# Performance work log

Hardware: AMD Instinct MI355X
Metric: run time of the kernel (lower is better)

Reference implementation:

```python
import jax, jax.numpy as jnp
import numpy as np

V, E, EH, H = 32000, 512, 1024, 512  # vocab, emb_dim, enc_hidden, dec_hidden
B, S = 16, 128


def setup_inputs() -> dict:
    key = jax.random.key(0)
    ks = jax.random.split(key, 8)
    g = lambda k, shape, scale: (jax.random.normal(k, shape, jnp.float32) * scale)
    return {
        "y": jax.random.randint(ks[0], (B, S), 0, V),
        "hn": jax.random.normal(ks[1], (B, 1, EH), jnp.float32),
        "emb": g(ks[2], (V, E), 0.02),          # embedding table
        "W_ih": g(ks[3], (3 * H, E), 0.05),      # GRU input weights (r,z,n)
        "W_hh": g(ks[4], (3 * H, H), 0.05),      # GRU hidden weights (r,z,n)
        "b_ih": jnp.zeros((3 * H,), jnp.float32),
        "b_hh": jnp.zeros((3 * H,), jnp.float32),
        "fc_w": g(ks[5], (H, EH), 0.03),         # fc: enc_hidden -> dec_hidden
        "fc_b": jnp.zeros((H,), jnp.float32),
        "pred_w": g(ks[6], (V, H), 0.03),        # pred: dec_hidden -> vocab
        "pred_b": jnp.zeros((V,), jnp.float32),
    }


def gru_scan(x, h0, W_ih, W_hh, b_ih, b_hh):
    """Single-layer unidirectional GRU (PyTorch gate order r,z,n).
    x: [B,S,E], h0: [B,H] -> outputs [B,S,H]."""
    h_dim = h0.shape[-1]
    # precompute input projections for all timesteps: [B,S,3H]
    gx = jnp.einsum('bse,ge->bsg', x, W_ih) + b_ih
    Wr, Wz, Wn = W_hh[:h_dim], W_hh[h_dim:2 * h_dim], W_hh[2 * h_dim:]
    br, bz, bn = b_hh[:h_dim], b_hh[h_dim:2 * h_dim], b_hh[2 * h_dim:]

    def step(h, g):
        gr, gz, gn = g[:, :h_dim], g[:, h_dim:2 * h_dim], g[:, 2 * h_dim:]
        r = jax.nn.sigmoid(gr + h @ Wr.T + br)
        z = jax.nn.sigmoid(gz + h @ Wz.T + bz)
        n = jnp.tanh(gn + r * (h @ Wn.T + bn))
        h_new = (1.0 - z) * n + z * h
        return h_new, h_new

    _, outs = jax.lax.scan(step, h0, jnp.swapaxes(gx, 0, 1))  # [S,B,H]
    return jnp.swapaxes(outs, 0, 1)  # [B,S,H]


def reference(y, hn, emb, W_ih, W_hh, b_ih, b_hh, fc_w, fc_b, pred_w, pred_b):
    # hn: [B,1,EH] -> fc -> [B,1,H] -> permute(1,0,2) -> initial hidden [B,H]
    h0 = (hn @ fc_w.T + fc_b)[:, 0, :]
    x = emb[y]  # [B,S,E]; dropout is identity in eval mode
    out = gru_scan(x, h0, W_ih, W_hh, b_ih, b_hh)  # [B,S,H]
    return out @ pred_w.T + pred_b  # [B,S,V]
```

## Files before the change

kernel.cpp:

```cpp
#include <hip/hip_runtime.h>


typedef __attribute__((ext_vector_type(8))) short           bf8_t;
typedef __attribute__((ext_vector_type(8))) unsigned short  us8_t;
typedef __attribute__((ext_vector_type(4))) unsigned short  us4_t;
typedef __attribute__((ext_vector_type(4))) float           f4_t;
typedef __attribute__((ext_vector_type(4))) unsigned int    u4_t;

#define SENT 0xFFFFFFFFu

__device__ __forceinline__ unsigned short f2bf(float x) {
    unsigned u = __builtin_bit_cast(unsigned, x);
    u += 0x7FFFu + ((u >> 16) & 1u);
    return (unsigned short)(u >> 16);
}
__device__ __forceinline__ float bf2f(unsigned short h) {
    unsigned u = (unsigned)h << 16;
    return __builtin_bit_cast(float, u);
}
__device__ __forceinline__ float sigm(float x) { return 1.0f / (1.0f + __expf(-x)); }

__device__ __forceinline__ void llc_store_f32(float* p, float v) {
    asm volatile("global_store_dword %0, %1, off sc0 sc1" :: "v"(p), "v"(v) : "memory");
}

__global__ void k_fill(unsigned int* __restrict__ p) {
    int i = blockIdx.x * blockDim.x + threadIdx.x;
    u4_t v = {SENT, SENT, SENT, SENT};
    ((u4_t*)p)[i] = v;
}

__global__ void k_conv(const float* __restrict__ src, unsigned short* __restrict__ dst, int n4) {
    int i = blockIdx.x * blockDim.x + threadIdx.x;
    int stride = gridDim.x * blockDim.x;
    for (; i < n4; i += stride) {
        f4_t v = ((const f4_t*)src)[i];
        us4_t o;
        o[0] = f2bf(v[0]); o[1] = f2bf(v[1]); o[2] = f2bf(v[2]); o[3] = f2bf(v[3]);
        ((us4_t*)dst)[i] = o;
    }
}

__global__ void k_gather(const int* __restrict__ y, const float* __restrict__ emb,
                         unsigned short* __restrict__ xbf) {
    int m = blockIdx.x;
    int row = y[m];
    int t = threadIdx.x;
    f4_t v = ((const f4_t*)(emb + (size_t)row * 512))[t];
    us4_t o;
    o[0] = f2bf(v[0]); o[1] = f2bf(v[1]); o[2] = f2bf(v[2]); o[3] = f2bf(v[3]);
    ((us4_t*)(xbf + (size_t)m * 512))[t] = o;
}

__global__ void k_h0(const float* __restrict__ hn, const float* __restrict__ fc_w,
                     const float* __restrict__ fc_b, float* __restrict__ h0) {
    __shared__ float sh[1024];
    int b = blockIdx.x, t = threadIdx.x;
    for (int i = t; i < 1024; i += 256) sh[i] = hn[b * 1024 + i];
    __syncthreads();
    int j = t;
    float a0 = fc_b[j], a1 = fc_b[j + 256];
    const float* w0 = fc_w + (size_t)j * 1024;
    const float* w1 = fc_w + (size_t)(j + 256) * 1024;
    #pragma unroll 8
    for (int e = 0; e < 1024; e++) { float he = sh[e]; a0 += he * w0[e]; a1 += he * w1[e]; }
    h0[b * 512 + j] = a0;
    h0[b * 512 + j + 256] = a1;
}

__launch_bounds__(256)
__global__ void k_gemm(const unsigned short* __restrict__ A, const unsigned short* __restrict__ Bt,
                       const float* __restrict__ bias, float* __restrict__ C, int N) {
    __shared__ unsigned short sA[128 * 64];
    __shared__ unsigned short sB[128 * 64];
    const int m0 = blockIdx.y * 128, n0 = blockIdx.x * 128;
    const int tid = threadIdx.x, lane = tid & 63, wave = tid >> 6;
    const int wm = wave >> 1, wn = wave & 1;
    f4_t acc[4][4] = {};
    for (int ks = 0; ks < 8; ks++) {
        const int k0 = ks * 64;
        #pragma unroll
        for (int t = 0; t < 4; t++) {
            int idx = tid + t * 256;
            int row = idx >> 3, slot = idx & 7;
            int sw = ((slot ^ (row & 7)) << 3);
            *(us8_t*)(&sA[row * 64 + sw]) = *(const us8_t*)(A + (size_t)(m0 + row) * 512 + k0 + slot * 8);
            *(us8_t*)(&sB[row * 64 + sw]) = *(const us8_t*)(Bt + (size_t)(n0 + row) * 512 + k0 + slot * 8);
        }
        __syncthreads();
        #pragma unroll
        for (int kk = 0; kk < 2; kk++) {
            bf8_t af[4], bfr[4];
            #pragma unroll
            for (int mi = 0; mi < 4; mi++) {
                int row = wm * 64 + mi * 16 + (lane & 15);
                int slot = (kk * 4 + (lane >> 4)) ^ (row & 7);
                af[mi] = *(const bf8_t*)(&sA[row * 64 + slot * 8]);
            }
            #pragma unroll
            for (int ni = 0; ni < 4; ni++) {
                int row = wn * 64 + ni * 16 + (lane & 15);
                int slot = (kk * 4 + (lane >> 4)) ^ (row & 7);
                bfr[ni] = *(const bf8_t*)(&sB[row * 64 + slot * 8]);
            }
            #pragma unroll
            for (int mi = 0; mi < 4; mi++)
                #pragma unroll
                for (int ni = 0; ni < 4; ni++)
                    acc[mi][ni] = __builtin_amdgcn_mfma_f32_16x16x32_bf16(af[mi], bfr[ni], acc[mi][ni], 0, 0, 0);
        }
        __syncthreads();
    }
    #pragma unroll
    for (int ni = 0; ni < 4; ni++) {
        int col = n0 + wn * 64 + ni * 16 + (lane & 15);
        float bv = bias[col];
        #pragma unroll
        for (int mi = 0; mi < 4; mi++) {
            int rbase = m0 + wm * 64 + mi * 16 + (lane >> 4) * 4;
            #pragma unroll
            for (int r = 0; r < 4; r++)
                C[(size_t)(rbase + r) * N + col] = acc[mi][ni][r] + bv;
        }
    }
}

__launch_bounds__(512, 1)
__global__ void k_rec(const float* __restrict__ W_hh, const float* __restrict__ b_hh,
                      const float* __restrict__ gx, float* __restrict__ hbuf,
                      unsigned short* __restrict__ Hout) {
    const int kb = blockIdx.x;
    const int j0 = kb * 32;
    const int tid = threadIdx.x, lane = tid & 63, wave = tid >> 6;
    __shared__ unsigned short sHi[16 * 512];
    __shared__ unsigned short sLo[16 * 512];
    __shared__ float sPre[96 * 17];

    bf8_t wfrag[16];
    if (wave < 6) {
        const int gate = wave >> 1, sub = wave & 1;
        const int wrow = gate * 512 + j0 + sub * 16 + (lane & 15);
        const f4_t* wp4 = (const f4_t*)(W_hh + (size_t)wrow * 512);
        #pragma unroll
        for (int kk = 0; kk < 16; kk++) {
            f4_t v0 = wp4[kk * 8 + (lane >> 4) * 2];
            f4_t v1 = wp4[kk * 8 + (lane >> 4) * 2 + 1];
            bf8_t f;
            f[0] = (short)f2bf(v0[0]); f[1] = (short)f2bf(v0[1]);
            f[2] = (short)f2bf(v0[2]); f[3] = (short)f2bf(v0[3]);
            f[4] = (short)f2bf(v1[0]); f[5] = (short)f2bf(v1[1]);
            f[6] = (short)f2bf(v1[2]); f[7] = (short)f2bf(v1[3]);
            wfrag[kk] = f;
        }
    }

    const int b_ = tid >> 5, jj = tid & 31;
    const float brv = b_hh[j0 + jj], bzv = b_hh[512 + j0 + jj], bnv = b_hh[1024 + j0 + jj];
    float h_reg = hbuf[b_ * 512 + j0 + jj];

    for (int s = 1; s <= 128; s++) {
        const float* gxp = gx + (size_t)(b_ * 128 + (s - 1)) * 1536 + j0 + jj;
        float gr = gxp[0], gz = gxp[512], gn = gxp[1024];

        const float* hsrc = hbuf + (size_t)(s - 1) * 8192;
        const float* p0 = hsrc + (size_t)tid * 4;
        const float* p1 = hsrc + (size_t)(tid + 512) * 4;
        const float* p2 = hsrc + (size_t)(tid + 1024) * 4;
        const float* p3 = hsrc + (size_t)(tid + 1536) * 4;
        f4_t hv0, hv1, hv2, hv3;
        int spins = 0;
        bool ok;
        do {
            asm volatile(
                "global_load_dwordx4 %0, %4, off sc0 sc1\n\t"
                "global_load_dwordx4 %1, %5, off sc0 sc1\n\t"
                "global_load_dwordx4 %2, %6, off sc0 sc1\n\t"
                "global_load_dwordx4 %3, %7, off sc0 sc1\n\t"
                "s_waitcnt vmcnt(0)"
                : "=&v"(hv0), "=&v"(hv1), "=&v"(hv2), "=&v"(hv3)
                : "v"(p0), "v"(p1), "v"(p2), "v"(p3)
                : "memory");
            ok = true;
            #pragma unroll
            for (int i = 0; i < 4; i++) {
                ok = ok && (__builtin_bit_cast(unsigned, hv0[i]) != SENT)
                        && (__builtin_bit_cast(unsigned, hv1[i]) != SENT)
                        && (__builtin_bit_cast(unsigned, hv2[i]) != SENT)
                        && (__builtin_bit_cast(unsigned, hv3[i]) != SENT);
            }
        } while (!ok && ++spins < (1 << 20));
        __builtin_amdgcn_sched_barrier(0);

        {
            f4_t hv[4] = {hv0, hv1, hv2, hv3};
            #pragma unroll
            for (int t = 0; t < 4; t++) {
                int idx4 = tid + t * 512;
                int row = idx4 >> 7, c4 = idx4 & 127;
                us4_t hi, lo;
                #pragma unroll
                for (int i = 0; i < 4; i++) {
                    unsigned short h = f2bf(hv[t][i]);
                    hi[i] = h;
                    lo[i] = f2bf(hv[t][i] - bf2f(h));
                }
                int base = row * 512 + (((c4 >> 1) ^ (row & 7)) << 3) + (c4 & 1) * 4;
                *(us4_t*)(&sHi[base]) = hi;
                *(us4_t*)(&sLo[base]) = lo;
            }
        }
        __syncthreads();

        if (wave < 6) {
            f4_t acc = {0.f, 0.f, 0.f, 0.f};
            const int m = lane & 15;
            #pragma unroll
            for (int kk = 0; kk < 16; kk++) {
                int off = m * 512 + (((kk * 4 + (lane >> 4)) ^ (m & 7)) << 3);
                bf8_t ahi = *(const bf8_t*)(&sHi[off]);
                bf8_t alo = *(const bf8_t*)(&sLo[off]);
                acc = __builtin_amdgcn_mfma_f32_16x16x32_bf16(ahi, wfrag[kk], acc, 0, 0, 0);
                acc = __builtin_amdgcn_mfma_f32_16x16x32_bf16(alo, wfrag[kk], acc, 0, 0, 0);
            }
            const int n = wave * 16 + (lane & 15);
            #pragma unroll
            for (int r = 0; r < 4; r++) sPre[n * 17 + (lane >> 4) * 4 + r] = acc[r];
        }
        __syncthreads();

        float r = sigm(gr + sPre[jj * 17 + b_] + brv);
        float z = sigm(gz + sPre[(32 + jj) * 17 + b_] + bzv);
        float nn = tanhf(gn + r * (sPre[(64 + jj) * 17 + b_] + bnv));
        float hnew = (1.f - z) * nn + z * h_reg;
        h_reg = hnew;

        llc_store_f32(&hbuf[(size_t)s * 8192 + b_ * 512 + j0 + jj], hnew);
        Hout[(size_t)(b_ * 128 + (s - 1)) * 512 + j0 + jj] = f2bf(hnew);
    }
}

extern "C" void kernel_launch(void* const* d_in, const int* in_sizes, int n_in,
                              void* d_out, int out_size, void* d_ws, size_t ws_size,
                              hipStream_t stream) {
    const int*   y      = (const int*)  d_in[0];
    const float* hn     = (const float*)d_in[1];
    const float* emb    = (const float*)d_in[2];
    const float* W_ih   = (const float*)d_in[3];
    const float* W_hh   = (const float*)d_in[4];
    const float* b_ih   = (const float*)d_in[5];
    const float* b_hh   = (const float*)d_in[6];
    const float* fc_w   = (const float*)d_in[7];
    const float* fc_b   = (const float*)d_in[8];
    const float* pred_w = (const float*)d_in[9];
    const float* pred_b = (const float*)d_in[10];
    float* out = (float*)d_out;

    char* ws = (char*)d_ws;
    size_t off = 0;
    auto alloc = [&](size_t bytes) { void* p = ws + off; off = (off + bytes + 255) & ~(size_t)255; return p; };
    float*          hbuf   = (float*)          alloc((size_t)129 * 8192 * 4);
    float*          gx     = (float*)          alloc((size_t)2048 * 1536 * 4);
    unsigned short* Hout   = (unsigned short*) alloc((size_t)2048 * 512 * 2);
    unsigned short* xbf    = (unsigned short*) alloc((size_t)2048 * 512 * 2);
    unsigned short* wihbf  = (unsigned short*) alloc((size_t)1536 * 512 * 2);
    unsigned short* pwbf   = (unsigned short*) alloc((size_t)32000 * 512 * 2);
    (void)ws_size; (void)in_sizes; (void)n_in; (void)out_size;

    k_fill  <<<1032, 256, 0, stream>>>((unsigned int*)hbuf);
    k_conv  <<<4096, 256, 0, stream>>>(pred_w, pwbf, 32000 * 512 / 4);
    k_conv  <<<512,  256, 0, stream>>>(W_ih,  wihbf, 1536 * 512 / 4);
    k_gather<<<2048, 128, 0, stream>>>(y, emb, xbf);
    k_h0    <<<16,   256, 0, stream>>>(hn, fc_w, fc_b, hbuf);
    dim3 gG(12, 16);
    k_gemm  <<<gG, 256, 0, stream>>>(xbf, wihbf, b_ih, gx, 1536);
    k_rec   <<<16, 512, 0, stream>>>(W_hh, b_hh, gx, hbuf, Hout);
    dim3 gP(250, 16);
    k_gemm  <<<gP, 256, 0, stream>>>(Hout, pwbf, pred_b, out, 32000);
}
```

Before: 572.5 us.

## Fuse all three GRU gates per wave and compute gate math in MFMA registers

Each of the first two waves now holds the r, z and n weight fragments for its 16 hidden columns and issues all six MFMA chains itself, so gate nonlinearities and the hidden update run directly on accumulator registers. This drops the sPre shared buffer and the shared-memory round trip that fed the gate math. It also prefetches the next step's gx values during the current step. The cost is that only 2 waves do the matmul instead of 6, which serialises six times more MFMAs per wave on the critical path and raises register pressure from the three fragment arrays.

```diff
diff --git a/kernel.cpp b/kernel.cpp
--- a/kernel.cpp
+++ b/kernel.cpp
@@ -19,6 +19,15 @@
     return __builtin_bit_cast(float, u);
 }
 __device__ __forceinline__ float sigm(float x) { return 1.0f / (1.0f + __expf(-x)); }
+
+__device__ __forceinline__ bf8_t mk_frag(f4_t v0, f4_t v1) {
+    bf8_t f;
+    f[0] = (short)f2bf(v0[0]); f[1] = (short)f2bf(v0[1]);
+    f[2] = (short)f2bf(v0[2]); f[3] = (short)f2bf(v0[3]);
+    f[4] = (short)f2bf(v1[0]); f[5] = (short)f2bf(v1[1]);
+    f[6] = (short)f2bf(v1[2]); f[7] = (short)f2bf(v1[3]);
+    return f;
+}
 
 __device__ __forceinline__ void llc_store_f32(float* p, float v) {
     asm volatile("global_store_dword %0, %1, off sc0 sc1" :: "v"(p), "v"(v) : "memory");
@@ -134,34 +143,38 @@
     const int tid = threadIdx.x, lane = tid & 63, wave = tid >> 6;
     __shared__ unsigned short sHi[16 * 512];
     __shared__ unsigned short sLo[16 * 512];
-    __shared__ float sPre[96 * 17];
-
-    bf8_t wfrag[16];
-    if (wave < 6) {
-        const int gate = wave >> 1, sub = wave & 1;
-        const int wrow = gate * 512 + j0 + sub * 16 + (lane & 15);
-        const f4_t* wp4 = (const f4_t*)(W_hh + (size_t)wrow * 512);
+
+    const bool comp = (wave < 2);
+    const int cidx = j0 + wave * 16 + (lane & 15);
+    const int bbase = (lane >> 4) * 4;
+
+    bf8_t wfR[16], wfZ[16], wfN[16];
+    float brv = 0.f, bzv = 0.f, bnv = 0.f;
+    f4_t h_reg = {0.f, 0.f, 0.f, 0.f};
+    float gxv[3][4];
+    if (comp) {
+        const f4_t* wr = (const f4_t*)(W_hh + (size_t)cidx * 512);
+        const f4_t* wz = (const f4_t*)(W_hh + (size_t)(512 + cidx) * 512);
+        const f4_t* wn = (const f4_t*)(W_hh + (size_t)(1024 + cidx) * 512);
+        const int fo = (lane >> 4) * 2;
         #pragma unroll
         for (int kk = 0; kk < 16; kk++) {
-            f4_t v0 = wp4[kk * 8 + (lane >> 4) * 2];
-            f4_t v1 = wp4[kk * 8 + (lane >> 4) * 2 + 1];
-            bf8_t f;
-            f[0] = (short)f2bf(v0[0]); f[1] = (short)f2bf(v0[1]);
-            f[2] = (short)f2bf(v0[2]); f[3] = (short)f2bf(v0[3]);
-            f[4] = (short)f2bf(v1[0]); f[5] = (short)f2bf(v1[1]);
-            f[6] = (short)f2bf(v1[2]); f[7] = (short)f2bf(v1[3]);
-            wfrag[kk] = f;
-        }
-    }
-
-    const int b_ = tid >> 5, jj = tid & 31;
-    const float brv = b_hh[j0 + jj], bzv = b_hh[512 + j0 + jj], bnv = b_hh[1024 + j0 + jj];
-    float h_reg = hbuf[b_ * 512 + j0 + jj];
+            wfR[kk] = mk_frag(wr[kk * 8 + fo], wr[kk * 8 + fo + 1]);
+            wfZ[kk] = mk_frag(wz[kk * 8 + fo], wz[kk * 8 + fo + 1]);
+            wfN[kk] = mk_frag(wn[kk * 8 + fo], wn[kk * 8 + fo + 1]);
+        }
+        brv = b_hh[cidx]; bzv = b_hh[512 + cidx]; bnv = b_hh[1024 + cidx];
+        #pragma unroll
+        for (int r = 0; r < 4; r++)
+            h_reg[r] = hbuf[(bbase + r) * 512 + cidx];
+        #pragma unroll
+        for (int g = 0; g < 3; g++)
+            #pragma unroll
+            for (int r = 0; r < 4; r++)
+                gxv[g][r] = gx[(size_t)((bbase + r) * 128) * 1536 + g * 512 + cidx];
+    }
 
     for (int s = 1; s <= 128; s++) {
-        const float* gxp = gx + (size_t)(b_ * 128 + (s - 1)) * 1536 + j0 + jj;
-        float gr = gxp[0], gz = gxp[512], gn = gxp[1024];
-
         const float* hsrc = hbuf + (size_t)(s - 1) * 8192;
         const float* p0 = hsrc + (size_t)tid * 4;
         const float* p1 = hsrc + (size_t)(tid + 512) * 4;
@@ -191,6 +204,16 @@
         } while (!ok && ++spins < (1 << 20));
         __builtin_amdgcn_sched_barrier(0);
 
+        float gnx[3][4];
+        if (comp) {
+            const int si = (s < 128) ? s : 127;
+            #pragma unroll
+            for (int g = 0; g < 3; g++)
+                #pragma unroll
+                for (int r = 0; r < 4; r++)
+                    gnx[g][r] = gx[(size_t)((bbase + r) * 128 + si) * 1536 + g * 512 + cidx];
+        }
+
         {
             f4_t hv[4] = {hv0, hv1, hv2, hv3};
             #pragma unroll
@@ -211,31 +234,39 @@
         }
         __syncthreads();
 
-        if (wave < 6) {
-            f4_t acc = {0.f, 0.f, 0.f, 0.f};
+        if (comp) {
+            f4_t aR = {}, aZ = {}, aN = {}, cR = {}, cZ = {}, cN = {};
             const int m = lane & 15;
             #pragma unroll
             for (int kk = 0; kk < 16; kk++) {
                 int off = m * 512 + (((kk * 4 + (lane >> 4)) ^ (m & 7)) << 3);
                 bf8_t ahi = *(const bf8_t*)(&sHi[off]);
                 bf8_t alo = *(const bf8_t*)(&sLo[off]);
-                acc = __builtin_amdgcn_mfma_f32_16x16x32_bf16(ahi, wfrag[kk], acc, 0, 0, 0);
-                acc = __builtin_amdgcn_mfma_f32_16x16x32_bf16(alo, wfrag[kk], acc, 0, 0, 0);
-            }
-            const int n = wave * 16 + (lane & 15);
-            #pragma unroll
-            for (int r = 0; r < 4; r++) sPre[n * 17 + (lane >> 4) * 4 + r] = acc[r];
+                aR = __builtin_amdgcn_mfma_f32_16x16x32_bf16(ahi, wfR[kk], aR, 0, 0, 0);
+                aZ = __builtin_amdgcn_mfma_f32_16x16x32_bf16(ahi, wfZ[kk], aZ, 0, 0, 0);
+                aN = __builtin_amdgcn_mfma_f32_16x16x32_bf16(ahi, wfN[kk], aN, 0, 0, 0);
+                cR = __builtin_amdgcn_mfma_f32_16x16x32_bf16(alo, wfR[kk], cR, 0, 0, 0);
+                cZ = __builtin_amdgcn_mfma_f32_16x16x32_bf16(alo, wfZ[kk], cZ, 0, 0, 0);
+                cN = __builtin_amdgcn_mfma_f32_16x16x32_bf16(alo, wfN[kk], cN, 0, 0, 0);
+            }
+            #pragma unroll
+            for (int r = 0; r < 4; r++) {
+                const int b = bbase + r;
+                float rr = sigm(gxv[0][r] + (aR[r] + cR[r]) + brv);
+                float zz = sigm(gxv[1][r] + (aZ[r] + cZ[r]) + bzv);
+                float nn = tanhf(gxv[2][r] + rr * ((aN[r] + cN[r]) + bnv));
+                float hnew = (1.f - zz) * nn + zz * h_reg[r];
+                h_reg[r] = hnew;
+                llc_store_f32(&hbuf[(size_t)s * 8192 + b * 512 + cidx], hnew);
+                Hout[(size_t)(b * 128 + (s - 1)) * 512 + cidx] = f2bf(hnew);
+            }
+            #pragma unroll
+            for (int g = 0; g < 3; g++)
+                #pragma unroll
+                for (int r = 0; r < 4; r++)
+                    gxv[g][r] = gnx[g][r];
         }
         __syncthreads();
-
-        float r = sigm(gr + sPre[jj * 17 + b_] + brv);
-        float z = sigm(gz + sPre[(32 + jj) * 17 + b_] + bzv);
-        float nn = tanhf(gn + r * (sPre[(64 + jj) * 17 + b_] + bnv));
-        float hnew = (1.f - z) * nn + z * h_reg;
-        h_reg = hnew;
-
-        llc_store_f32(&hbuf[(size_t)s * 8192 + b_ * 512 + j0 + jj], hnew);
-        Hout[(size_t)(b_ * 128 + (s - 1)) * 512 + j0 + jj] = f2bf(hnew);
     }
 }
 
```

Result: slower. 932.6 us (+62.9%).

## Restructure GRU recurrence to single-wave blocks exchanging packed bf16 hidden state

Applied to the files above, without the earlier changes.

The recurrent kernel changes from 16 blocks of 512 threads to 32 single-wave blocks. Each block owns 16 hidden columns for all three gates, and each wave loads the whole previous hidden state straight from global memory into MFMA fragments, so the LDS staging and both __syncthreads per step go away. The hidden state is now exchanged as packed bf16 pairs instead of fp32, which halves the polling traffic. The hi/lo split-precision MFMA is dropped, so the recurrent matmul runs in plain bf16. This cuts per-step latency in the sequential loop but lowers accuracy of the recurrent state.

```diff
diff --git a/kernel.cpp b/kernel.cpp
--- a/kernel.cpp
+++ b/kernel.cpp
@@ -14,13 +14,18 @@
     u += 0x7FFFu + ((u >> 16) & 1u);
     return (unsigned short)(u >> 16);
 }
-__device__ __forceinline__ float bf2f(unsigned short h) {
-    unsigned u = (unsigned)h << 16;
-    return __builtin_bit_cast(float, u);
-}
 __device__ __forceinline__ float sigm(float x) { return 1.0f / (1.0f + __expf(-x)); }
 
-__device__ __forceinline__ void llc_store_f32(float* p, float v) {
+__device__ __forceinline__ bf8_t mk_frag(f4_t v0, f4_t v1) {
+    bf8_t f;
+    f[0] = (short)f2bf(v0[0]); f[1] = (short)f2bf(v0[1]);
+    f[2] = (short)f2bf(v0[2]); f[3] = (short)f2bf(v0[3]);
+    f[4] = (short)f2bf(v1[0]); f[5] = (short)f2bf(v1[1]);
+    f[6] = (short)f2bf(v1[2]); f[7] = (short)f2bf(v1[3]);
+    return f;
+}
+
+__device__ __forceinline__ void llc_store_u32(unsigned int* p, unsigned int v) {
     asm volatile("global_store_dword %0, %1, off sc0 sc1" :: "v"(p), "v"(v) : "memory");
 }
 
@@ -53,7 +58,7 @@
 }
 
 __global__ void k_h0(const float* __restrict__ hn, const float* __restrict__ fc_w,
-                     const float* __restrict__ fc_b, float* __restrict__ h0) {
+                     const float* __restrict__ fc_b, float* __restrict__ h0m) {
     __shared__ float sh[1024];
     int b = blockIdx.x, t = threadIdx.x;
     for (int i = t; i < 1024; i += 256) sh[i] = hn[b * 1024 + i];
@@ -64,8 +69,8 @@
     const float* w1 = fc_w + (size_t)(j + 256) * 1024;
     #pragma unroll 8
     for (int e = 0; e < 1024; e++) { float he = sh[e]; a0 += he * w0[e]; a1 += he * w1[e]; }
-    h0[b * 512 + j] = a0;
-    h0[b * 512 + j + 256] = a1;
+    h0m[b * 512 + j] = a0;
+    h0m[b * 512 + j + 256] = a1;
 }
 
 __launch_bounds__(256)
@@ -125,117 +130,112 @@
     }
 }
 
-__launch_bounds__(512, 1)
+__launch_bounds__(64, 1)
 __global__ void k_rec(const float* __restrict__ W_hh, const float* __restrict__ b_hh,
-                      const float* __restrict__ gx, float* __restrict__ hbuf,
-                      unsigned short* __restrict__ Hout) {
-    const int kb = blockIdx.x;
-    const int j0 = kb * 32;
-    const int tid = threadIdx.x, lane = tid & 63, wave = tid >> 6;
-    __shared__ unsigned short sHi[16 * 512];
-    __shared__ unsigned short sLo[16 * 512];
-    __shared__ float sPre[96 * 17];
-
-    bf8_t wfrag[16];
-    if (wave < 6) {
-        const int gate = wave >> 1, sub = wave & 1;
-        const int wrow = gate * 512 + j0 + sub * 16 + (lane & 15);
-        const f4_t* wp4 = (const f4_t*)(W_hh + (size_t)wrow * 512);
+                      const float* __restrict__ gx, const float* __restrict__ h0m,
+                      unsigned int* __restrict__ hbuf, unsigned short* __restrict__ Hout) {
+    const int c = blockIdx.x;
+    const int lane = threadIdx.x;
+    const int col = c * 16 + (lane & 15);
+    const int kgrp = lane >> 4;
+    const int bbase = kgrp * 4;
+
+    bf8_t wfR[16], wfZ[16], wfN[16];
+    {
+        const f4_t* wr = (const f4_t*)(W_hh + (size_t)col * 512);
+        const f4_t* wz = (const f4_t*)(W_hh + (size_t)(512 + col) * 512);
+        const f4_t* wn = (const f4_t*)(W_hh + (size_t)(1024 + col) * 512);
+        const int fo = kgrp * 2;
         #pragma unroll
         for (int kk = 0; kk < 16; kk++) {
-            f4_t v0 = wp4[kk * 8 + (lane >> 4) * 2];
-            f4_t v1 = wp4[kk * 8 + (lane >> 4) * 2 + 1];
-            bf8_t f;
-            f[0] = (short)f2bf(v0[0]); f[1] = (short)f2bf(v0[1]);
-            f[2] = (short)f2bf(v0[2]); f[3] = (short)f2bf(v0[3]);
-            f[4] = (short)f2bf(v1[0]); f[5] = (short)f2bf(v1[1]);
-            f[6] = (short)f2bf(v1[2]); f[7] = (short)f2bf(v1[3]);
-            wfrag[kk] = f;
-        }
-    }
-
-    const int b_ = tid >> 5, jj = tid & 31;
-    const float brv = b_hh[j0 + jj], bzv = b_hh[512 + j0 + jj], bnv = b_hh[1024 + j0 + jj];
-    float h_reg = hbuf[b_ * 512 + j0 + jj];
+            wfR[kk] = mk_frag(wr[kk * 8 + fo], wr[kk * 8 + fo + 1]);
+            wfZ[kk] = mk_frag(wz[kk * 8 + fo], wz[kk * 8 + fo + 1]);
+            wfN[kk] = mk_frag(wn[kk * 8 + fo], wn[kk * 8 + fo + 1]);
+        }
+    }
+    const float brv = b_hh[col], bzv = b_hh[512 + col], bnv = b_hh[1024 + col];
+
+    f4_t h_reg;
+    #pragma unroll
+    for (int r = 0; r < 4; r++) h_reg[r] = h0m[(bbase + r) * 512 + col];
+
+    #pragma unroll
+    for (int r = 0; r < 4; r++) {
+        unsigned int hb = f2bf(h_reg[r]);
+        unsigned int pr = __shfl_xor(hb, 1, 64);
+        if (!(lane & 1))
+            llc_store_u32(&hbuf[(bbase + r) * 256 + (col >> 1)], hb | (pr << 16));
+    }
 
     for (int s = 1; s <= 128; s++) {
-        const float* gxp = gx + (size_t)(b_ * 128 + (s - 1)) * 1536 + j0 + jj;
-        float gr = gxp[0], gz = gxp[512], gn = gxp[1024];
-
-        const float* hsrc = hbuf + (size_t)(s - 1) * 8192;
-        const float* p0 = hsrc + (size_t)tid * 4;
-        const float* p1 = hsrc + (size_t)(tid + 512) * 4;
-        const float* p2 = hsrc + (size_t)(tid + 1024) * 4;
-        const float* p3 = hsrc + (size_t)(tid + 1536) * 4;
-        f4_t hv0, hv1, hv2, hv3;
+        float gxr[4], gxz[4], gxn[4];
+        #pragma unroll
+        for (int r = 0; r < 4; r++) {
+            const float* gp = gx + (size_t)((bbase + r) * 128 + (s - 1)) * 1536 + col;
+            gxr[r] = gp[0]; gxz[r] = gp[512]; gxn[r] = gp[1024];
+        }
+
+        const unsigned int* base = hbuf + (size_t)(s - 1) * 4096 + (lane & 15) * 256 + kgrp * 4;
+        u4_t q[16];
         int spins = 0;
         bool ok;
         do {
             asm volatile(
-                "global_load_dwordx4 %0, %4, off sc0 sc1\n\t"
-                "global_load_dwordx4 %1, %5, off sc0 sc1\n\t"
-                "global_load_dwordx4 %2, %6, off sc0 sc1\n\t"
-                "global_load_dwordx4 %3, %7, off sc0 sc1\n\t"
+                "global_load_dwordx4 %0,  %16, off sc0 sc1\n\t"
+                "global_load_dwordx4 %1,  %16, off offset:64 sc0 sc1\n\t"
+                "global_load_dwordx4 %2,  %16, off offset:128 sc0 sc1\n\t"
+                "global_load_dwordx4 %3,  %16, off offset:192 sc0 sc1\n\t"
+                "global_load_dwordx4 %4,  %16, off offset:256 sc0 sc1\n\t"
+                "global_load_dwordx4 %5,  %16, off offset:320 sc0 sc1\n\t"
+                "global_load_dwordx4 %6,  %16, off offset:384 sc0 sc1\n\t"
+                "global_load_dwordx4 %7,  %16, off offset:448 sc0 sc1\n\t"
+                "global_load_dwordx4 %8,  %16, off offset:512 sc0 sc1\n\t"
+                "global_load_dwordx4 %9,  %16, off offset:576 sc0 sc1\n\t"
+                "global_load_dwordx4 %10, %16, off offset:640 sc0 sc1\n\t"
+                "global_load_dwordx4 %11, %16, off offset:704 sc0 sc1\n\t"
+                "global_load_dwordx4 %12, %16, off offset:768 sc0 sc1\n\t"
+                "global_load_dwordx4 %13, %16, off offset:832 sc0 sc1\n\t"
+                "global_load_dwordx4 %14, %16, off offset:896 sc0 sc1\n\t"
+                "global_load_dwordx4 %15, %16, off offset:960 sc0 sc1\n\t"
                 "s_waitcnt vmcnt(0)"
-                : "=&v"(hv0), "=&v"(hv1), "=&v"(hv2), "=&v"(hv3)
-                : "v"(p0), "v"(p1), "v"(p2), "v"(p3)
+                : "=&v"(q[0]), "=&v"(q[1]), "=&v"(q[2]), "=&v"(q[3]),
+                  "=&v"(q[4]), "=&v"(q[5]), "=&v"(q[6]), "=&v"(q[7]),
+                  "=&v"(q[8]), "=&v"(q[9]), "=&v"(q[10]), "=&v"(q[11]),
+                  "=&v"(q[12]), "=&v"(q[13]), "=&v"(q[14]), "=&v"(q[15])
+                : "v"(base)
                 : "memory");
             ok = true;
             #pragma unroll
-            for (int i = 0; i < 4; i++) {
-                ok = ok && (__builtin_bit_cast(unsigned, hv0[i]) != SENT)
-                        && (__builtin_bit_cast(unsigned, hv1[i]) != SENT)
-                        && (__builtin_bit_cast(unsigned, hv2[i]) != SENT)
-                        && (__builtin_bit_cast(unsigned, hv3[i]) != SENT);
-            }
-        } while (!ok && ++spins < (1 << 20));
+            for (int kk = 0; kk < 16; kk++)
+                #pragma unroll
+                for (int i = 0; i < 4; i++)
+                    ok = ok && (q[kk][i] != SENT);
+        } while (!__all(ok) && ++spins < (1 << 20));
         __builtin_amdgcn_sched_barrier(0);
 
-        {
-            f4_t hv[4] = {hv0, hv1, hv2, hv3};
-            #pragma unroll
-            for (int t = 0; t < 4; t++) {
-                int idx4 = tid + t * 512;
-                int row = idx4 >> 7, c4 = idx4 & 127;
-                us4_t hi, lo;
-                #pragma unroll
-                for (int i = 0; i < 4; i++) {
-                    unsigned short h = f2bf(hv[t][i]);
-                    hi[i] = h;
-                    lo[i] = f2bf(hv[t][i] - bf2f(h));
-                }
-                int base = row * 512 + (((c4 >> 1) ^ (row & 7)) << 3) + (c4 & 1) * 4;
-                *(us4_t*)(&sHi[base]) = hi;
-                *(us4_t*)(&sLo[base]) = lo;
-            }
-        }
-        __syncthreads();
-
-        if (wave < 6) {
-            f4_t acc = {0.f, 0.f, 0.f, 0.f};
-            const int m = lane & 15;
-            #pragma unroll
-            for (int kk = 0; kk < 16; kk++) {
-                int off = m * 512 + (((kk * 4 + (lane >> 4)) ^ (m & 7)) << 3);
-                bf8_t ahi = *(const bf8_t*)(&sHi[off]);
-                bf8_t alo = *(const bf8_t*)(&sLo[off]);
-                acc = __builtin_amdgcn_mfma_f32_16x16x32_bf16(ahi, wfrag[kk], acc, 0, 0, 0);
-                acc = __builtin_amdgcn_mfma_f32_16x16x32_bf16(alo, wfrag[kk], acc, 0, 0, 0);
-            }
-            const int n = wave * 16 + (lane & 15);
-            #pragma unroll
-            for (int r = 0; r < 4; r++) sPre[n * 17 + (lane >> 4) * 4 + r] = acc[r];
-        }
-        __syncthreads();
-
-        float r = sigm(gr + sPre[jj * 17 + b_] + brv);
-        float z = sigm(gz + sPre[(32 + jj) * 17 + b_] + bzv);
-        float nn = tanhf(gn + r * (sPre[(64 + jj) * 17 + b_] + bnv));
-        float hnew = (1.f - z) * nn + z * h_reg;
-        h_reg = hnew;
-
-        llc_store_f32(&hbuf[(size_t)s * 8192 + b_ * 512 + j0 + jj], hnew);
-        Hout[(size_t)(b_ * 128 + (s - 1)) * 512 + j0 + jj] = f2bf(hnew);
+        f4_t aR = {}, aZ = {}, aN = {};
+        #pragma unroll
+        for (int kk = 0; kk < 16; kk++) {
+            bf8_t af = __builtin_bit_cast(bf8_t, q[kk]);
+            aR = __builtin_amdgcn_mfma_f32_16x16x32_bf16(af, wfR[kk], aR, 0, 0, 0);
+            aZ = __builtin_amdgcn_mfma_f32_16x16x32_bf16(af, wfZ[kk], aZ, 0, 0, 0);
+            aN = __builtin_amdgcn_mfma_f32_16x16x32_bf16(af, wfN[kk], aN, 0, 0, 0);
+        }
+
+        #pragma unroll
+        for (int r = 0; r < 4; r++) {
+            const int b = bbase + r;
+            float rr = sigm(gxr[r] + aR[r] + brv);
+            float zz = sigm(gxz[r] + aZ[r] + bzv);
+            float nn = tanhf(gxn[r] + rr * (aN[r] + bnv));
+            float hnew = (1.f - zz) * nn + zz * h_reg[r];
+            h_reg[r] = hnew;
+            unsigned int hb = f2bf(hnew);
+            Hout[(size_t)(b * 128 + (s - 1)) * 512 + col] = (unsigned short)hb;
+            unsigned int pr = __shfl_xor(hb, 1, 64);
+            if (!(lane & 1))
+                llc_store_u32(&hbuf[(size_t)s * 4096 + b * 256 + (col >> 1)], hb | (pr << 16));
+        }
     }
 }
 
@@ -258,7 +258,8 @@
     char* ws = (char*)d_ws;
     size_t off = 0;
     auto alloc = [&](size_t bytes) { void* p = ws + off; off = (off + bytes + 255) & ~(size_t)255; return p; };
-    float*          hbuf   = (float*)          alloc((size_t)129 * 8192 * 4);
+    unsigned int*   hbuf   = (unsigned int*)   alloc((size_t)129 * 4096 * 4);
+    float*          h0m    = (float*)          alloc((size_t)16 * 512 * 4);
     float*          gx     = (float*)          alloc((size_t)2048 * 1536 * 4);
     unsigned short* Hout   = (unsigned short*) alloc((size_t)2048 * 512 * 2);
     unsigned short* xbf    = (unsigned short*) alloc((size_t)2048 * 512 * 2);
@@ -266,14 +267,14 @@
     unsigned short* pwbf   = (unsigned short*) alloc((size_t)32000 * 512 * 2);
     (void)ws_size; (void)in_sizes; (void)n_in; (void)out_size;
 
-    k_fill  <<<1032, 256, 0, stream>>>((unsigned int*)hbuf);
+    k_fill  <<<516,  256, 0, stream>>>(hbuf);
     k_conv  <<<4096, 256, 0, stream>>>(pred_w, pwbf, 32000 * 512 / 4);
     k_conv  <<<512,  256, 0, stream>>>(W_ih,  wihbf, 1536 * 512 / 4);
     k_gather<<<2048, 128, 0, stream>>>(y, emb, xbf);
-    k_h0    <<<16,   256, 0, stream>>>(hn, fc_w, fc_b, hbuf);
+    k_h0    <<<16,   256, 0, stream>>>(hn, fc_w, fc_b, h0m);
     dim3 gG(12, 16);
     k_gemm  <<<gG, 256, 0, stream>>>(xbf, wihbf, b_ih, gx, 1536);
-    k_rec   <<<16, 512, 0, stream>>>(W_hh, b_hh, gx, hbuf, Hout);
+    k_rec   <<<32, 64, 0, stream>>>(W_hh, b_hh, gx, h0m, hbuf, Hout);
     dim3 gP(250, 16);
     k_gemm  <<<gP, 256, 0, stream>>>(Hout, pwbf, pred_b, out, 32000);
 }
```

After: 790.0 us. 1.38x slower.
